# Kernel tuning notes

Measured on AMD Instinct MI355X. Metric: run time of the kernel, lower is better.

## Reference

```python
import jax, jax.numpy as jnp
import numpy as np

EPS = 1e-5


def _conv3x3(x, w):
    # x: [B,C,H,W], w: [O,I,3,3], stride 1, padding 1
    return jax.lax.conv_general_dilated(
        x, w, window_strides=(1, 1), padding=((1, 1), (1, 1)),
        dimension_numbers=("NCHW", "OIHW", "NCHW"))


def _bn(x, g, b, m, v):
    # inference-mode BatchNorm2d over channel dim
    inv = jax.lax.rsqrt(v + EPS) * g
    return x * inv[None, :, None, None] + (b - m * inv)[None, :, None, None]


def setup_inputs() -> dict:
    key = jax.random.key(0)
    B, C, H, W = 32, 256, 56, 56
    ks = jax.random.split(key, 16)
    x = jax.random.normal(ks[0], (B, C, H, W), dtype=jnp.float32)
    mask = (jax.random.uniform(ks[1], (B, 1, H, W)) < 0.5).astype(jnp.float32)
    # dilated mask = 3x3 max-pool of mask
    mask_dilate = jax.lax.reduce_window(
        mask, -jnp.inf, jax.lax.max, (1, 1, 3, 3), (1, 1, 1, 1), "SAME")
    mask_dilate = jnp.maximum(mask_dilate, 0.0).astype(jnp.float32)
    vector = (jax.random.uniform(ks[2], (B, C)) < 0.5).astype(jnp.float32)
    conv1_w = jax.random.normal(ks[3], (C, C, 3, 3), dtype=jnp.float32) * 0.05
    conv2_w = jax.random.normal(ks[4], (C, C, 3, 3), dtype=jnp.float32) * 0.05
    bn1_g = 1.0 + 0.1 * jax.random.normal(ks[5], (C,), dtype=jnp.float32)
    bn1_b = 0.1 * jax.random.normal(ks[6], (C,), dtype=jnp.float32)
    bn1_m = 0.1 * jax.random.normal(ks[7], (C,), dtype=jnp.float32)
    bn1_v = 0.5 + jax.random.uniform(ks[8], (C,), dtype=jnp.float32)
    bn2_g = 1.0 + 0.1 * jax.random.normal(ks[9], (C,), dtype=jnp.float32)
    bn2_b = 0.1 * jax.random.normal(ks[10], (C,), dtype=jnp.float32)
    bn2_m = 0.1 * jax.random.normal(ks[11], (C,), dtype=jnp.float32)
    bn2_v = 0.5 + jax.random.uniform(ks[12], (C,), dtype=jnp.float32)
    return dict(x=x, mask=mask, mask_dilate=mask_dilate, vector=vector,
                conv1_w=conv1_w, bn1_g=bn1_g, bn1_b=bn1_b, bn1_m=bn1_m, bn1_v=bn1_v,
                conv2_w=conv2_w, bn2_g=bn2_g, bn2_b=bn2_b, bn2_m=bn2_m, bn2_v=bn2_v)


def reference(x, mask, mask_dilate, vector,
              conv1_w, bn1_g, bn1_b, bn1_m, bn1_v,
              conv2_w, bn2_g, bn2_b, bn2_m, bn2_v):
    # Sparse BasicBlock, stride=1, no downsample, input_mask=True.
    identity = x
    h = x * mask_dilate                      # apply_mask(x, mask_dilate)
    h = _conv3x3(h, conv1_w) * mask          # conv3x3_mask(conv1, ...)
    h = jax.nn.relu(_bn(h, bn1_g, bn1_b, bn1_m, bn1_v)) * mask_dilate  # bn_relu_mask(bn1, relu, ., mask_dilate)
    h = h * mask                             # apply_mask(x, mask)
    h = h * vector[:, :, None, None]         # channel_process(x, vector)
    h = _conv3x3(h, conv2_w) * mask          # conv3x3_mask(conv2, ...)
    h = _bn(h, bn2_g, bn2_b, bn2_m, bn2_v) * mask  # bn_relu_mask(bn2, None, ., mask)
    out = identity + h * mask                # identity + apply_mask(x, mask)
    return jax.nn.relu(out)
```

## Files before the change

### kernel.cpp

```cpp
#include <hip/hip_runtime.h>
#include <cstdint>


#define EPS 1e-5f

constexpr int Cc = 256, Hh = 56, Ww = 56, HW = 3136;
constexpr int NG = 16;
constexpr int PH = 58, PW = 66;
constexpr int PS = PH * PW * 8;
constexpr int IPS = 32 * PS;
constexpr int WP_EL = 16 * 9 * 2 * 256 * 8;
constexpr int PACK_POS = NG * 32 * PH * PW;

typedef __bf16 bf16x8 __attribute__((ext_vector_type(8)));
typedef __bf16 bf16x4 __attribute__((ext_vector_type(4)));
typedef float  f32x16 __attribute__((ext_vector_type(16)));

__global__ void pack_xm2(const float* __restrict__ x, const float* __restrict__ md,
                         __bf16* __restrict__ dst, int img0) {
    int pos = blockIdx.x * 256 + threadIdx.x;
    int xx = pos % PW; int t = pos / PW;
    int yy = t % PH;  t /= PH;
    int ci8 = t & 31; int il = t >> 5;
    int img = img0 + il;
    bf16x8 v = {};
    int xi = xx - 1, yi = yy - 1;
    if ((unsigned)xi < 56u && (unsigned)yi < 56u) {
        float mdv = md[(size_t)img * HW + yi * 56 + xi];
        #pragma unroll
        for (int j = 0; j < 8; ++j)
            v[j] = (__bf16)(x[((size_t)(img * Cc) + ci8 * 8 + j) * HW + yi * 56 + xi] * mdv);
    }
    *(bf16x8*)&dst[(size_t)pos * 8] = v;
}

__global__ void zero_fill(__bf16* __restrict__ dst) {
    int pos = blockIdx.x * 256 + threadIdx.x;
    bf16x8 z = {};
    *(bf16x8*)&dst[(size_t)pos * 8] = z;
}

__global__ void pack_w(const float* __restrict__ w1, const float* __restrict__ w2,
                       __bf16* __restrict__ wp1, __bf16* __restrict__ wp2) {
    int id = blockIdx.x * 256 + threadIdx.x;
    const float* w = blockIdx.y ? w2 : w1;
    __bf16* wp = blockIdx.y ? wp2 : wp1;
    int j = id & 7; int t = id >> 3;
    int co = t & 255; t >>= 8;
    int half = t & 1; t >>= 1;
    int tap = t % 9; int chunk = t / 9;
    int ci = chunk * 16 + half * 8 + j;
    wp[id] = (__bf16)(w[((size_t)co * Cc + ci) * 9 + tap]);
}

__global__ void bn_prep(const float* g1, const float* b1, const float* m1, const float* v1,
                        const float* g2, const float* b2, const float* m2, const float* v2,
                        float* binv1, float* bbeta1, float* binv2, float* bbeta2) {
    int c = threadIdx.x;
    float i1 = g1[c] * rsqrtf(v1[c] + EPS);
    binv1[c] = i1; bbeta1[c] = b1[c] - m1[c] * i1;
    float i2 = g2[c] * rsqrtf(v2[c] + EPS);
    binv2[c] = i2; bbeta2[c] = b2[c] - m2[c] * i2;
}

template <bool C1>
__global__ __launch_bounds__(256, 2)
void conv_kern(const __bf16* __restrict__ pix,
               const __bf16* __restrict__ wp,
               const float* __restrict__ maskg,
               const float* __restrict__ vec,
               const float* __restrict__ binv, const float* __restrict__ bbeta,
               const float* __restrict__ xin,
               void* __restrict__ dstv, int img0) {
    const int tid = threadIdx.x;
    const int lane = tid & 63, wave = tid >> 6;
    const int xlane = lane & 31, halfid = lane >> 5;
    const int band = blockIdx.x, cob = blockIdx.y, il = blockIdx.z;
    const int img = img0 + il;
    const int ybase = band * 4 + 2 * (wave >> 1);
    const int c0 = cob * 128 + (wave & 1) * 64;

    f32x16 acc[2][4];
    #pragma unroll
    for (int m = 0; m < 2; ++m)
        #pragma unroll
        for (int it = 0; it < 4; ++it)
            #pragma unroll
            for (int r = 0; r < 16; ++r) acc[m][it][r] = 0.f;

    const __bf16* pimg = pix + (size_t)il * IPS;

    for (int chunk = 0; chunk < 16; ++chunk) {
        const __bf16* wch = wp + (size_t)chunk * (9 * 2 * 256 * 8);
        const __bf16* pch = pimg + (size_t)(chunk * 2 + halfid) * PS;
        #pragma unroll
        for (int kh = 0; kh < 3; ++kh) {
            #pragma unroll
            for (int kw = 0; kw < 3; ++kw) {
                const int tap = kh * 3 + kw;
                bf16x8 wf[2], pf[4];
                #pragma unroll
                for (int m = 0; m < 2; ++m)
                    wf[m] = *(const bf16x8*)&wch[((size_t)(tap * 2 + halfid) * 256 +
                                                  c0 + m * 32 + xlane) * 8];
                #pragma unroll
                for (int it = 0; it < 4; ++it) {
                    int row = ybase + (it >> 1) + kh;
                    int col = (it & 1) * 32 + kw + xlane;
                    pf[it] = *(const bf16x8*)&pch[((size_t)row * PW + col) * 8];
                }
                #pragma unroll
                for (int m = 0; m < 2; ++m)
                    #pragma unroll
                    for (int it = 0; it < 4; ++it)
                        acc[m][it] = __builtin_amdgcn_mfma_f32_32x32x16_bf16(
                            wf[m], pf[it], acc[m][it], 0, 0, 0);
            }
        }
    }

    float mv[4]; int yv[4], xv[4]; bool okv[4];
    #pragma unroll
    for (int it = 0; it < 4; ++it) {
        yv[it] = ybase + (it >> 1);
        xv[it] = (it & 1) * 32 + xlane;
        okv[it] = xv[it] < 56;
        mv[it] = okv[it] ? maskg[(size_t)img * HW + yv[it] * 56 + xv[it]] : 0.f;
    }

    if constexpr (C1) {
        __bf16* u2 = (__bf16*)dstv;
        #pragma unroll
        for (int m = 0; m < 2; ++m)
            #pragma unroll
            for (int rg = 0; rg < 4; ++rg) {
                const int c4 = c0 + m * 32 + rg * 8 + 4 * halfid;
                const float4 iv4 = *(const float4*)&binv[c4];
                const float4 bt4 = *(const float4*)&bbeta[c4];
                const float4 vv4 = *(const float4*)&vec[img * Cc + c4];
                const float ivv[4] = {iv4.x, iv4.y, iv4.z, iv4.w};
                const float btv[4] = {bt4.x, bt4.y, bt4.z, bt4.w};
                const float vvv[4] = {vv4.x, vv4.y, vv4.z, vv4.w};
                const int co8 = (c0 + m * 32) / 8 + rg;
                #pragma unroll
                for (int it = 0; it < 4; ++it) {
                    if (okv[it]) {
                        bf16x4 h;
                        #pragma unroll
                        for (int j = 0; j < 4; ++j) {
                            float o = fmaxf(fmaf(acc[m][it][rg * 4 + j], ivv[j], btv[j]), 0.f)
                                      * mv[it] * vvv[j];
                            h[j] = (__bf16)o;
                        }
                        size_t a = (((size_t)(il * 32 + co8) * PH + (yv[it] + 1)) * PW +
                                    (xv[it] + 1)) * 8 + 4 * halfid;
                        *(bf16x4*)&u2[a] = h;
                    }
                }
            }
    } else {
        float* outp = (float*)dstv;
        #pragma unroll
        for (int m = 0; m < 2; ++m)
            #pragma unroll
            for (int rg = 0; rg < 4; ++rg) {
                const int c4 = c0 + m * 32 + rg * 8 + 4 * halfid;
                const float4 iv4 = *(const float4*)&binv[c4];
                const float4 bt4 = *(const float4*)&bbeta[c4];
                const float ivv[4] = {iv4.x, iv4.y, iv4.z, iv4.w};
                const float btv[4] = {bt4.x, bt4.y, bt4.z, bt4.w};
                #pragma unroll
                for (int j = 0; j < 4; ++j) {
                    const size_t cbase = (size_t)(img * Cc + c4 + j) * HW;
                    #pragma unroll
                    for (int it = 0; it < 4; ++it) {
                        if (okv[it]) {
                            size_t oa = cbase + yv[it] * 56 + xv[it];
                            float o = fmaxf(
                                xin[oa] + mv[it] * fmaf(acc[m][it][rg * 4 + j], ivv[j], btv[j]),
                                0.f);
                            outp[oa] = o;
                        }
                    }
                }
            }
    }
}

extern "C" void kernel_launch(void* const* d_in, const int* in_sizes, int n_in,
                              void* d_out, int out_size, void* d_ws, size_t ws_size,
                              hipStream_t stream) {
    const float* x    = (const float*)d_in[0];
    const float* mask = (const float*)d_in[1];
    const float* md   = (const float*)d_in[2];
    const float* vec  = (const float*)d_in[3];
    const float* w1   = (const float*)d_in[4];
    const float* bn1g = (const float*)d_in[5];
    const float* bn1b = (const float*)d_in[6];
    const float* bn1m = (const float*)d_in[7];
    const float* bn1v = (const float*)d_in[8];
    const float* w2   = (const float*)d_in[9];
    const float* bn2g = (const float*)d_in[10];
    const float* bn2b = (const float*)d_in[11];
    const float* bn2m = (const float*)d_in[12];
    const float* bn2v = (const float*)d_in[13];
    float* out = (float*)d_out;

    __bf16* xm2 = (__bf16*)d_ws;
    __bf16* u2  = xm2 + (size_t)NG * IPS;
    __bf16* wp1 = u2 + (size_t)NG * IPS;
    __bf16* wp2 = wp1 + WP_EL;
    float* binv1  = (float*)(wp2 + WP_EL);
    float* bbeta1 = binv1 + 256;
    float* binv2  = bbeta1 + 256;
    float* bbeta2 = binv2 + 256;

    pack_w<<<dim3(WP_EL / 256, 2), dim3(256), 0, stream>>>(w1, w2, wp1, wp2);
    bn_prep<<<dim3(1), dim3(256), 0, stream>>>(bn1g, bn1b, bn1m, bn1v,
                                               bn2g, bn2b, bn2m, bn2v,
                                               binv1, bbeta1, binv2, bbeta2);

    for (int g = 0; g < 2; ++g) {
        const int img0 = g * NG;
        pack_xm2<<<dim3(PACK_POS / 256), dim3(256), 0, stream>>>(x, md, xm2, img0);
        zero_fill<<<dim3(PACK_POS / 256), dim3(256), 0, stream>>>(u2);
        dim3 grid(14, 2, NG);
        conv_kern<true><<<grid, dim3(256), 0, stream>>>(
            xm2, wp1, mask, vec, binv1, bbeta1, nullptr, u2, img0);
        conv_kern<false><<<grid, dim3(256), 0, stream>>>(
            u2, wp2, mask, nullptr, binv2, bbeta2, x, out, img0);
    }
}
```

Measured before the change: 592.1 us.

## Drop padded layout, reuse pixel rows across kernel taps, batch all images

The halo-padded bf16 staging buffers and the zero_fill pass are replaced by an unpadded planar layout. Out-of-bounds taps are now handled with predicated loads that substitute zeros. The conv inner loop is reordered to iterate kw outermost, loading four input rows once and reusing them across the three kh taps. This cuts pixel fragment loads per chunk. The two 16-image groups are merged into one launch per stage, which doubles the grid and removes several kernel launches, at the cost of extra bounds-check arithmetic and more register pressure.

```diff
diff --git a/kernel.cpp b/kernel.cpp
--- a/kernel.cpp
+++ b/kernel.cpp
@@ -4,40 +4,24 @@
 
 #define EPS 1e-5f
 
-constexpr int Cc = 256, Hh = 56, Ww = 56, HW = 3136;
-constexpr int NG = 16;
-constexpr int PH = 58, PW = 66;
-constexpr int PS = PH * PW * 8;
-constexpr int IPS = 32 * PS;
+constexpr int Bn = 32, Cc = 256, Hh = 56, Ww = 56, HW = 3136;
 constexpr int WP_EL = 16 * 9 * 2 * 256 * 8;
-constexpr int PACK_POS = NG * 32 * PH * PW;
 
 typedef __bf16 bf16x8 __attribute__((ext_vector_type(8)));
 typedef __bf16 bf16x4 __attribute__((ext_vector_type(4)));
 typedef float  f32x16 __attribute__((ext_vector_type(16)));
 
-__global__ void pack_xm2(const float* __restrict__ x, const float* __restrict__ md,
-                         __bf16* __restrict__ dst, int img0) {
+__global__ void pack_xm(const float* __restrict__ x, const float* __restrict__ md,
+                        __bf16* __restrict__ dst) {
     int pos = blockIdx.x * 256 + threadIdx.x;
-    int xx = pos % PW; int t = pos / PW;
-    int yy = t % PH;  t /= PH;
-    int ci8 = t & 31; int il = t >> 5;
-    int img = img0 + il;
-    bf16x8 v = {};
-    int xi = xx - 1, yi = yy - 1;
-    if ((unsigned)xi < 56u && (unsigned)yi < 56u) {
-        float mdv = md[(size_t)img * HW + yi * 56 + xi];
-        #pragma unroll
-        for (int j = 0; j < 8; ++j)
-            v[j] = (__bf16)(x[((size_t)(img * Cc) + ci8 * 8 + j) * HW + yi * 56 + xi] * mdv);
-    }
+    int pxl = pos % HW; int q = pos / HW;
+    int ci8 = q & 31, img = q >> 5;
+    float mdv = md[(size_t)img * HW + pxl];
+    bf16x8 v;
+    #pragma unroll
+    for (int j = 0; j < 8; ++j)
+        v[j] = (__bf16)(x[((size_t)(img * Cc) + ci8 * 8 + j) * HW + pxl] * mdv);
     *(bf16x8*)&dst[(size_t)pos * 8] = v;
-}
-
-__global__ void zero_fill(__bf16* __restrict__ dst) {
-    int pos = blockIdx.x * 256 + threadIdx.x;
-    bf16x8 z = {};
-    *(bf16x8*)&dst[(size_t)pos * 8] = z;
 }
 
 __global__ void pack_w(const float* __restrict__ w1, const float* __restrict__ w2,
@@ -71,12 +55,11 @@
                const float* __restrict__ vec,
                const float* __restrict__ binv, const float* __restrict__ bbeta,
                const float* __restrict__ xin,
-               void* __restrict__ dstv, int img0) {
+               void* __restrict__ dstv) {
     const int tid = threadIdx.x;
     const int lane = tid & 63, wave = tid >> 6;
     const int xlane = lane & 31, halfid = lane >> 5;
-    const int band = blockIdx.x, cob = blockIdx.y, il = blockIdx.z;
-    const int img = img0 + il;
+    const int band = blockIdx.x, cob = blockIdx.y, img = blockIdx.z;
     const int ybase = band * 4 + 2 * (wave >> 1);
     const int c0 = cob * 128 + (wave & 1) * 64;
 
@@ -88,34 +71,43 @@
             #pragma unroll
             for (int r = 0; r < 16; ++r) acc[m][it][r] = 0.f;
 
-    const __bf16* pimg = pix + (size_t)il * IPS;
+    const __bf16* pimg = pix + (size_t)img * (32 * HW * 8);
+    const bf16x8 zf = {};
 
     for (int chunk = 0; chunk < 16; ++chunk) {
         const __bf16* wch = wp + (size_t)chunk * (9 * 2 * 256 * 8);
-        const __bf16* pch = pimg + (size_t)(chunk * 2 + halfid) * PS;
-        #pragma unroll
-        for (int kh = 0; kh < 3; ++kh) {
-            #pragma unroll
-            for (int kw = 0; kw < 3; ++kw) {
-                const int tap = kh * 3 + kw;
-                bf16x8 wf[2], pf[4];
+        const __bf16* pch = pimg + (size_t)(chunk * 2 + halfid) * (HW * 8);
+        #pragma unroll
+        for (int kw = 0; kw < 3; ++kw) {
+            bf16x8 wf[3][2], pf[4][2];
+            #pragma unroll
+            for (int kh = 0; kh < 3; ++kh)
                 #pragma unroll
                 for (int m = 0; m < 2; ++m)
-                    wf[m] = *(const bf16x8*)&wch[((size_t)(tap * 2 + halfid) * 256 +
-                                                  c0 + m * 32 + xlane) * 8];
-                #pragma unroll
-                for (int it = 0; it < 4; ++it) {
-                    int row = ybase + (it >> 1) + kh;
-                    int col = (it & 1) * 32 + kw + xlane;
-                    pf[it] = *(const bf16x8*)&pch[((size_t)row * PW + col) * 8];
+                    wf[kh][m] = *(const bf16x8*)&wch[
+                        ((size_t)((kh * 3 + kw) * 2 + halfid) * 256 +
+                         c0 + m * 32 + xlane) * 8];
+            #pragma unroll
+            for (int rr = 0; rr < 4; ++rr)
+                #pragma unroll
+                for (int xh = 0; xh < 2; ++xh) {
+                    const int r = ybase - 1 + rr;
+                    const int c = xh * 32 + xlane + kw - 1;
+                    const bool ok = ((unsigned)r < 56u) & ((unsigned)c < 56u);
+                    const size_t a = ok ? (size_t)(r * Ww + c) * 8 : 0;
+                    bf16x8 v = *(const bf16x8*)&pch[a];
+                    pf[rr][xh] = ok ? v : zf;
                 }
+            #pragma unroll
+            for (int kh = 0; kh < 3; ++kh)
                 #pragma unroll
                 for (int m = 0; m < 2; ++m)
                     #pragma unroll
-                    for (int it = 0; it < 4; ++it)
-                        acc[m][it] = __builtin_amdgcn_mfma_f32_32x32x16_bf16(
-                            wf[m], pf[it], acc[m][it], 0, 0, 0);
-            }
+                    for (int orow = 0; orow < 2; ++orow)
+                        #pragma unroll
+                        for (int xh = 0; xh < 2; ++xh)
+                            acc[m][orow * 2 + xh] = __builtin_amdgcn_mfma_f32_32x32x16_bf16(
+                                wf[kh][m], pf[orow + kh][xh], acc[m][orow * 2 + xh], 0, 0, 0);
         }
     }
 
@@ -129,7 +121,7 @@
     }
 
     if constexpr (C1) {
-        __bf16* u2 = (__bf16*)dstv;
+        __bf16* u = (__bf16*)dstv;
         #pragma unroll
         for (int m = 0; m < 2; ++m)
             #pragma unroll
@@ -152,9 +144,9 @@
                                       * mv[it] * vvv[j];
                             h[j] = (__bf16)o;
                         }
-                        size_t a = (((size_t)(il * 32 + co8) * PH + (yv[it] + 1)) * PW +
-                                    (xv[it] + 1)) * 8 + 4 * halfid;
-                        *(bf16x4*)&u2[a] = h;
+                        size_t a = ((size_t)(img * 32 + co8) * HW +
+                                    yv[it] * 56 + xv[it]) * 8 + 4 * halfid;
+                        *(bf16x4*)&u[a] = h;
                     }
                 }
             }
@@ -206,9 +198,10 @@
     const float* bn2v = (const float*)d_in[13];
     float* out = (float*)d_out;
 
-    __bf16* xm2 = (__bf16*)d_ws;
-    __bf16* u2  = xm2 + (size_t)NG * IPS;
-    __bf16* wp1 = u2 + (size_t)NG * IPS;
+    const size_t planar = (size_t)Bn * 32 * HW * 8;
+    __bf16* xm  = (__bf16*)d_ws;
+    __bf16* u   = xm + planar;
+    __bf16* wp1 = u + planar;
     __bf16* wp2 = wp1 + WP_EL;
     float* binv1  = (float*)(wp2 + WP_EL);
     float* bbeta1 = binv1 + 256;
@@ -219,15 +212,11 @@
     bn_prep<<<dim3(1), dim3(256), 0, stream>>>(bn1g, bn1b, bn1m, bn1v,
                                                bn2g, bn2b, bn2m, bn2v,
                                                binv1, bbeta1, binv2, bbeta2);
-
-    for (int g = 0; g < 2; ++g) {
-        const int img0 = g * NG;
-        pack_xm2<<<dim3(PACK_POS / 256), dim3(256), 0, stream>>>(x, md, xm2, img0);
-        zero_fill<<<dim3(PACK_POS / 256), dim3(256), 0, stream>>>(u2);
-        dim3 grid(14, 2, NG);
-        conv_kern<true><<<grid, dim3(256), 0, stream>>>(
-            xm2, wp1, mask, vec, binv1, bbeta1, nullptr, u2, img0);
-        conv_kern<false><<<grid, dim3(256), 0, stream>>>(
-            u2, wp2, mask, nullptr, binv2, bbeta2, x, out, img0);
-    }
-}
+    pack_xm<<<dim3((Bn * 32 * HW) / 256), dim3(256), 0, stream>>>(x, md, xm);
+
+    dim3 grid(14, 2, Bn);
+    conv_kern<true><<<grid, dim3(256), 0, stream>>>(
+        xm, wp1, mask, vec, binv1, bbeta1, nullptr, u);
+    conv_kern<false><<<grid, dim3(256), 0, stream>>>(
+        u, wp2, mask, nullptr, binv2, bbeta2, x, out);
+}
```

New measurement: 611.4 us. 3.2% more time.
